# Kernel optimization log

Measured on AMD Instinct MI355X. Metric: run time of the kernel, lower is better.

The kernel has to match this reference:

```python
import jax, jax.numpy as jnp
import numpy as np

B, T, C = 2, 2048, 2048
H = 16          # n_head == n_kv_head
HD = 128        # head_size = hidden_dim // n_head (nope/value dim)
RD = 64         # qk_rope_head_dim
QLR = 1536      # q_lora_rank
KLR = 512       # kv_lora_rank
BASE = 10000.0
SCALE = (HD + RD) ** -0.5  # mscale = 1.0 since rope_scale = 1.0
EPS = 1e-6


def _rms(x, w):
    return x * jax.lax.rsqrt(jnp.mean(x * x, axis=-1, keepdims=True) + EPS) * w


def _rope_cos_sin(seq_len, dim):
    inv_freq = 1.0 / (BASE ** (jnp.arange(0, dim, 2, dtype=jnp.float32) / dim))
    t = jnp.arange(seq_len, dtype=jnp.float32)
    freqs = jnp.outer(t, inv_freq)            # [T, dim/2]
    emb = jnp.concatenate([freqs, freqs], -1)  # [T, dim]
    return jnp.cos(emb), jnp.sin(emb)


def _rotate_half(x):
    h = x.shape[-1] // 2
    return jnp.concatenate([-x[..., h:], x[..., :h]], axis=-1)


def setup_inputs() -> dict:
    key = jax.random.key(0)
    ks = jax.random.split(key, 8)
    s = 0.02
    return {
        "x": jax.random.normal(ks[0], (B, T, C), jnp.float32),
        "Wq_down": jax.random.normal(ks[1], (C, QLR), jnp.float32) * s,
        "q_norm_w": jnp.ones((QLR,), jnp.float32),
        "Wq_up": jax.random.normal(ks[2], (QLR, H * HD), jnp.float32) * s,
        "Wq_pe": jax.random.normal(ks[3], (QLR, H * RD), jnp.float32) * s,
        "Wkv_down": jax.random.normal(ks[4], (C, KLR), jnp.float32) * s,
        "kv_norm_w": jnp.ones((KLR,), jnp.float32),
        "Wkv_up": jax.random.normal(ks[5], (KLR, H * 2 * HD), jnp.float32) * s,
        "Wk_pe": jax.random.normal(ks[6], (C, RD), jnp.float32) * s,
        "k_pe_norm_w": jnp.ones((RD,), jnp.float32),
        "Wo": jax.random.normal(ks[7], (H * HD, C), jnp.float32) * s,
    }


def reference(x, Wq_down, q_norm_w, Wq_up, Wq_pe, Wkv_down, kv_norm_w,
              Wkv_up, Wk_pe, k_pe_norm_w, Wo):
    # ---- low-rank Q path ----
    cQ = _rms(x @ Wq_down, q_norm_w)                      # [B,T,QLR]
    q_nop = (cQ @ Wq_up).reshape(B, T, H, HD).transpose(0, 2, 1, 3)   # [B,H,T,HD]
    q_pe = (cQ @ Wq_pe).reshape(B, T, H, RD).transpose(0, 2, 1, 3)    # [B,H,T,RD]
    # ---- low-rank KV path ----
    cKV = _rms(x @ Wkv_down, kv_norm_w)                   # [B,T,KLR]
    kv = cKV @ Wkv_up                                     # [B,T,H*2*HD]
    k_nop, v = jnp.split(kv, 2, axis=-1)
    k_nop = k_nop.reshape(B, T, H, HD).transpose(0, 2, 1, 3)          # [B,H,T,HD]
    v = v.reshape(B, T, H, HD).transpose(0, 2, 1, 3)                  # [B,H,T,HD]
    # ---- decoupled RoPE key (shared across heads) ----
    k_pe = _rms(x @ Wk_pe, k_pe_norm_w).reshape(B, T, 1, RD).transpose(0, 2, 1, 3)  # [B,1,T,RD]
    cos, sin = _rope_cos_sin(T, RD)                       # [T,RD]
    q_pe = q_pe * cos + _rotate_half(q_pe) * sin
    k_pe = k_pe * cos + _rotate_half(k_pe) * sin
    # ---- concat nope + rope, causal SDPA ----
    q = jnp.concatenate([q_nop, q_pe], axis=-1)                           # [B,H,T,HD+RD]
    k = jnp.concatenate([k_nop, jnp.broadcast_to(k_pe, (B, H, T, RD))], axis=-1)
    scores = jnp.einsum('bhqd,bhkd->bhqk', q, k) * SCALE
    mask = jnp.tril(jnp.ones((T, T), dtype=bool))
    scores = jnp.where(mask, scores, jnp.finfo(scores.dtype).min)
    attn = jax.nn.softmax(scores, axis=-1)
    y = jnp.einsum('bhqk,bhkd->bhqd', attn, v)                            # [B,H,T,HD]
    y = y.transpose(0, 2, 1, 3).reshape(B, T, H * HD)
    return y @ Wo
```

## Files before the change

### kernel.cpp

```cpp
#include <hip/hip_runtime.h>
#include <hip/hip_bf16.h>
#include <cmath>

typedef __hip_bfloat16 bf16;
typedef __attribute__((ext_vector_type(8))) short s16x8;
typedef __attribute__((ext_vector_type(4))) float f32x4;

#define B_   2
#define T_   2048
#define C_   2048
#define H_   16
#define HD_  128
#define RD_  64
#define QLR_ 1536
#define KLR_ 512
#define SCALE_ 0.07216878364870322f

static __device__ __forceinline__ float b2f(bf16 v){ return __bfloat162float(v); }
static __device__ __forceinline__ bf16  f2b(float v){ return __float2bfloat16(v); }
static __device__ __forceinline__ float us2f(unsigned short u){
    union { unsigned short s[2]; float f; } v; v.s[0]=0; v.s[1]=u; return v.f;
}
static __device__ __forceinline__ float ldS(const void* p, size_t i, int isf32){
    return isf32 ? ((const float*)p)[i] : b2f(((const bf16*)p)[i]);
}
static __device__ __forceinline__ void ld4(const void* p, size_t i, int isf32, float* o){
    if (isf32) {
        float4 v = *(const float4*)((const float*)p + i);
        o[0]=v.x; o[1]=v.y; o[2]=v.z; o[3]=v.w;
    } else {
        ushort4 u = *(const ushort4*)((const bf16*)p + i);
        o[0]=us2f(u.x); o[1]=us2f(u.y); o[2]=us2f(u.z); o[3]=us2f(u.w);
    }
}

__global__ __launch_bounds__(64) void detect_kernel(const unsigned short* __restrict__ x,
                                                    int* __restrict__ flag)
{
    int big = 0;
    for (int i = threadIdx.x; i < 1024; i += 64) {
        const unsigned short u = x[2*i];
        const int e = (u >> 7) & 0xFF;
        if (e >= 139) big++;
    }
    #pragma unroll
    for (int off = 32; off; off >>= 1) big += __shfl_down(big, off, 64);
    if (threadIdx.x == 0) *flag = (big > 8) ? 1 : 0;
}

__global__ __launch_bounds__(256) void convert_kernel(const void* __restrict__ in,
                                                      bf16* __restrict__ out, int n,
                                                      const int* __restrict__ flag)
{
    const int f = *flag;
    const int i0 = (blockIdx.x * 256 + threadIdx.x) * 8;
    if (i0 >= n) return;
    float v[8];
    ld4(in, i0, f, v);
    ld4(in, i0 + 4, f, v + 4);
    bf16* o = out + i0;
    #pragma unroll
    for (int k = 0; k < 8; ++k) o[k] = f2b(v[k]);
}

struct TDesc { const void* in; bf16* out; int R, Cc, blkStart, nx; };
struct TBatch { TDesc d[5]; int nseg; };

__global__ __launch_bounds__(256) void transpose_batch(TBatch tb,
                                                       const int* __restrict__ flag)
{
    const int f = *flag;
    const int bid = blockIdx.x;
    int s = 0;
    #pragma unroll
    for (int i = 1; i < 5; ++i)
        if (i < tb.nseg && bid >= tb.d[i].blkStart) s = i;
    const TDesc d = tb.d[s];
    const int local = bid - d.blkStart;
    const int c0 = (local % d.nx) * 32;
    const int r0 = (local / d.nx) * 32;

    __shared__ float tile[32][33];
    const int tx = threadIdx.x & 31, ty = threadIdx.x >> 5;
    #pragma unroll
    for (int i = 0; i < 4; ++i)
        tile[ty + 8*i][tx] = ldS(d.in, (size_t)(r0 + ty + 8*i) * d.Cc + c0 + tx, f);
    __syncthreads();
    #pragma unroll
    for (int i = 0; i < 4; ++i)
        d.out[(size_t)(c0 + ty + 8*i) * d.R + r0 + tx] = f2b(tile[tx][ty + 8*i]);
}

__global__ __launch_bounds__(256) void transpose_v_kernel(const bf16* __restrict__ kvb,
                                                          bf16* __restrict__ vT)
{
    __shared__ bf16 tile[32][34];
    const int c0 = blockIdx.x * 32;
    const int r0 = blockIdx.y * 32;
    const int tx = threadIdx.x & 31, ty = threadIdx.x >> 5;
    #pragma unroll
    for (int i = 0; i < 4; ++i)
        tile[ty + 8*i][tx] = kvb[(size_t)(r0 + ty + 8*i) * (H_*256) + H_*128 + c0 + tx];
    __syncthreads();
    const int b  = r0 >> 11;
    const int t0 = r0 & (T_ - 1);
    #pragma unroll
    for (int i = 0; i < 4; ++i) {
        const int c  = c0 + ty + 8*i;
        const int hh = c >> 7, dd = c & 127;
        vT[(((size_t)b*H_ + hh)*HD_ + dd)*T_ + t0 + tx] = tile[tx][ty + 8*i];
    }
}

struct GOuts { void* p[3]; int start[3]; int stride[3]; int nseg; };

__global__ __launch_bounds__(256, 2) void mfma_gemm(const bf16* __restrict__ A,
                                                    const bf16* __restrict__ BT,
                                                    GOuts go, int N, int K,
                                                    const int* __restrict__ flag, int cH)
{
    __shared__ __align__(16) char smem[65536];
    const int cf   = cH ? *flag : 0;
    const int tid  = threadIdx.x;
    const int lane = tid & 63;
    const int quad = lane >> 4;
    const int l16  = lane & 15;
    const int w    = tid >> 6;
    const int wm   = w >> 1, wn = w & 1;
    const int bm   = blockIdx.y * 128, bn = blockIdx.x * 128;

    int seg = 0;
    #pragma unroll
    for (int i = 1; i < 3; ++i)
        if (i < go.nseg && bn >= go.start[i]) seg = i;
    void* const dstp   = go.p[seg];
    const int  dstoff  = go.start[seg];
    const int  dstride = go.stride[seg];

    const int nkt = K >> 6;

    const int sR   = tid >> 3;
    const int sCol = ((tid & 7) ^ (sR & 7)) * 8;
    const bf16* gA = A  + (size_t)(bm + sR) * K + sCol;
    const bf16* gB = BT + (size_t)(bn + sR) * K + sCol;
    const int rxk  = l16 & 7;
    const int aOff = (wm*64 + l16) * 128;
    const int bOff = 16384 + (wn*64 + l16) * 128;

    f32x4 acc[4][4];
    #pragma unroll
    for (int i = 0; i < 4; ++i)
        #pragma unroll
        for (int j = 0; j < 4; ++j)
            acc[i][j] = (f32x4){0.f, 0.f, 0.f, 0.f};

    s16x8 af[4][2], bf[4][2];

    #define STG(buf, kt) do {                                                    \
        const int ke_ = ((kt) < nkt ? (kt) : nkt-1) * 64;                        \
        _Pragma("unroll")                                                        \
        for (int j_ = 0; j_ < 4; ++j_)                                           \
            __builtin_amdgcn_global_load_lds(                                    \
                (const __attribute__((address_space(1))) unsigned int*)          \
                    (gA + (size_t)(j_*32) * K + ke_),                            \
                (__attribute__((address_space(3))) unsigned int*)                \
                    (smem + (buf)*32768 + j_*4096 + tid*16), 16, 0, 0);          \
        _Pragma("unroll")                                                        \
        for (int j_ = 0; j_ < 4; ++j_)                                           \
            __builtin_amdgcn_global_load_lds(                                    \
                (const __attribute__((address_space(1))) unsigned int*)          \
                    (gB + (size_t)(j_*32) * K + ke_),                            \
                (__attribute__((address_space(3))) unsigned int*)                \
                    (smem + (buf)*32768 + 16384 + j_*4096 + tid*16), 16, 0, 0);  \
    } while (0)

    #define LD(buf) do {                                                         \
        _Pragma("unroll")                                                        \
        for (int i_ = 0; i_ < 4; ++i_)                                           \
            _Pragma("unroll")                                                    \
            for (int ks_ = 0; ks_ < 2; ++ks_)                                    \
                af[i_][ks_] = *(const s16x8*)(smem + (buf)*32768 + aOff          \
                              + i_*2048 + ((((ks_<<2)|quad) ^ rxk) << 4));       \
        _Pragma("unroll")                                                        \
        for (int j_ = 0; j_ < 4; ++j_)                                           \
            _Pragma("unroll")                                                    \
            for (int ks_ = 0; ks_ < 2; ++ks_)                                    \
                bf[j_][ks_] = *(const s16x8*)(smem + (buf)*32768 + bOff          \
                              + j_*2048 + ((((ks_<<2)|quad) ^ rxk) << 4));       \
    } while (0)

    #define MM do {                                                              \
        __builtin_amdgcn_s_setprio(1);                                           \
        _Pragma("unroll")                                                        \
        for (int i_ = 0; i_ < 4; ++i_)                                           \
            _Pragma("unroll")                                                    \
            for (int j_ = 0; j_ < 4; ++j_)                                       \
                _Pragma("unroll")                                                \
                for (int ks_ = 0; ks_ < 2; ++ks_)                                \
                    acc[i_][j_] = __builtin_amdgcn_mfma_f32_16x16x32_bf16(       \
                        af[i_][ks_], bf[j_][ks_], acc[i_][j_], 0, 0, 0);         \
        __builtin_amdgcn_s_setprio(0);                                           \
    } while (0)

    #define DRAIN asm volatile("s_waitcnt vmcnt(0)" ::: "memory");               \
                  __builtin_amdgcn_s_barrier()

    STG(0, 0);
    DRAIN;

    for (int t = 0; t < nkt; t += 2) {
        STG(1, t+1);
        LD(0);
        MM;
        DRAIN;
        STG(0, t+2);
        LD(1);
        MM;
        DRAIN;
    }

    #undef STG
    #undef LD
    #undef MM
    #undef DRAIN

    #pragma unroll
    for (int i = 0; i < 4; ++i) {
        const int crow = bm + wm*64 + i*16 + quad*4;
        #pragma unroll
        for (int r = 0; r < 4; ++r) {
            #pragma unroll
            for (int j = 0; j < 4; ++j) {
                const int ccol = bn + wn*64 + j*16 + l16;
                if (ccol < N) {
                    const size_t idx = (size_t)(crow + r) * dstride + (ccol - dstoff);
                    if (cf) ((float*)dstp)[idx] = acc[i][j][r];
                    else    ((bf16*)dstp)[idx] = f2b(acc[i][j][r]);
                }
            }
        }
    }
}

template<int NPER>
__global__ __launch_bounds__(256) void rms_kernel(bf16* __restrict__ X,
                                                  const void* __restrict__ w,
                                                  const int* __restrict__ flag)
{
    const int wf = *flag;
    const int ncols = NPER * 256;
    __shared__ float red[4];
    const int row = blockIdx.x;
    const int tid = threadIdx.x;
    bf16* xr = X + (size_t)row * ncols;
    float vals[NPER];
    float ss = 0.f;
    #pragma unroll
    for (int i = 0; i < NPER; ++i) {
        float v = b2f(xr[tid + i*256]);
        vals[i] = v; ss += v*v;
    }
    #pragma unroll
    for (int off = 32; off; off >>= 1) ss += __shfl_down(ss, off, 64);
    if ((tid & 63) == 0) red[tid >> 6] = ss;
    __syncthreads();
    const float tot = red[0]+red[1]+red[2]+red[3];
    const float rs  = rsqrtf(tot / (float)ncols + 1e-6f);
    #pragma unroll
    for (int i = 0; i < NPER; ++i) {
        const int c = tid + i*256;
        xr[c] = f2b(vals[i] * rs * ldS(w, c, wf));
    }
}

__global__ __launch_bounds__(64) void kpe_rms_rope(bf16* __restrict__ X,
                                                   const void* __restrict__ w,
                                                   const int* __restrict__ flag)
{
    const int wf   = *flag;
    const int row  = blockIdx.x;
    const int t    = row & (T_ - 1);
    const int lane = threadIdx.x;
    bf16* xr = X + (size_t)row * RD_;
    const float v = b2f(xr[lane]);
    float ss = v * v;
    #pragma unroll
    for (int off = 32; off; off >>= 1) ss += __shfl_down(ss, off, 64);
    ss = __shfl(ss, 0, 64);
    const float rs = rsqrtf(ss / 64.f + 1e-6f);
    const float xn = v * rs * ldS(w, lane, wf);
    const int   i  = lane & 31;
    const float freq = powf(10000.f, -(float)(2*i) / 64.f);
    const float ang  = (float)t * freq;
    const float s = sinf(ang), c = cosf(ang);
    const float other = __shfl_xor(xn, 32, 64);
    const float o = (lane < 32) ? (xn * c - other * s) : (other * s + xn * c);
    xr[lane] = f2b(o);
}

__global__ __launch_bounds__(256) void qpe_rope(bf16* __restrict__ X)
{
    const int row = blockIdx.x;
    const int t   = row & (T_ - 1);
    bf16* xr = X + (size_t)row * (H_ * RD_);
    const int tid = threadIdx.x;
    #pragma unroll
    for (int pp = 0; pp < 2; ++pp) {
        const int p  = tid + pp * 256;
        const int hh = p >> 5;
        const int i  = p & 31;
        const int i0 = hh * 64 + i;
        const int i1 = i0 + 32;
        const float x1 = b2f(xr[i0]), x2 = b2f(xr[i1]);
        const float freq = powf(10000.f, -(float)(2*i) / 64.f);
        const float ang  = (float)t * freq;
        const float s = sinf(ang), c = cosf(ang);
        xr[i0] = f2b(x1 * c - x2 * s);
        xr[i1] = f2b(x1 * s + x2 * c);
    }
}

__global__ __launch_bounds__(256, 2) void flash_attn(const bf16* __restrict__ qnop,
                                                     const bf16* __restrict__ qpe,
                                                     const bf16* __restrict__ kv,
                                                     const bf16* __restrict__ kpe,
                                                     const bf16* __restrict__ vT,
                                                     bf16* __restrict__ y)
{
    __shared__ __align__(16) short Klds[64 * 192];
    __shared__ __align__(16) short Vt[128 * 64];
    __shared__ __align__(16) short Plds[4][16 * 64];

    const int h   = blockIdx.x;
    const int qt  = 31 - (int)blockIdx.y;
    const int b   = blockIdx.z;
    const int q0  = qt * 64;
    const int tid = threadIdx.x;
    const int w    = tid >> 6;
    const int lane = tid & 63;
    const int quad = lane >> 4;
    const int l16  = lane & 15;
    const int rk   = l16 & 7;
    const int rkp  = (l16 ^ (l16 >> 3)) & 7;
    const int row0 = q0 + w * 16;
    const size_t bT = (size_t)b * T_;
    const int bh  = b * H_ + h;

    const int kR = tid >> 4, kS = tid & 15;
    const int pR = tid >> 3, pS = tid & 7;
    const int vD = tid >> 3, vS = tid & 7;

    const bf16* gK = kv  + (bT + kR) * (H_*256) + h*128 + kS*8;
    const bf16* gP = kpe + (bT + pR) * RD_ + pS*8;
    const bf16* gV = vT  + ((size_t)bh*HD_ + vD) * T_ + vS*8;

    short* const wK = &Klds[kR*192 + ((kS ^ (kR & 7)) << 3)];
    short* const wP = &Klds[pR*192 + 128 + ((pS ^ (pR & 7)) << 3)];
    short* const wV = &Vt[vD*64 + ((vS ^ (vD & 7)) << 3)];

    s16x8 aq[6];
    {
        const size_t r = bT + row0 + l16;
        const bf16* qn = qnop + r * (H_*128) + h*128 + quad*8;
        #pragma unroll
        for (int kk = 0; kk < 4; ++kk) aq[kk] = *(const s16x8*)(qn + kk*32);
        const bf16* qp = qpe + r * (H_*64) + h*64 + quad*8;
        aq[4] = *(const s16x8*)(qp);
        aq[5] = *(const s16x8*)(qp + 32);
    }

    f32x4 o[8];
    #pragma unroll
    for (int i = 0; i < 8; ++i) o[i] = (f32x4){0.f,0.f,0.f,0.f};
    float m_run[4] = {-1e30f,-1e30f,-1e30f,-1e30f};
    float l_run[4] = {0.f,0.f,0.f,0.f};

    uint4 k0, k1, k2, k3, p0, p1, v0, v1, v2, v3;
    #define PF(J0) do {                                                     \
        const bf16* a_ = gK + (size_t)(J0) * (H_*256);                      \
        k0 = *(const uint4*)(a_);                                           \
        k1 = *(const uint4*)(a_ + 16*(H_*256));                             \
        k2 = *(const uint4*)(a_ + 32*(H_*256));                             \
        k3 = *(const uint4*)(a_ + 48*(H_*256));                             \
        const bf16* p_ = gP + (size_t)(J0) * RD_;                           \
        p0 = *(const uint4*)(p_);                                           \
        p1 = *(const uint4*)(p_ + 32*RD_);                                  \
        const bf16* v_ = gV + (J0);                                         \
        v0 = *(const uint4*)(v_);                                           \
        v1 = *(const uint4*)(v_ + 32*T_);                                   \
        v2 = *(const uint4*)(v_ + 64*T_);                                   \
        v3 = *(const uint4*)(v_ + 96*T_);                                   \
    } while (0)

    PF(0);

    const int ntiles = qt + 1;
    for (int it = 0; it < ntiles; ++it) {
        const int j0 = it * 64;
        asm volatile("s_waitcnt lgkmcnt(0)\n\ts_barrier" ::: "memory");

        *(uint4*)(wK)          = k0;
        *(uint4*)(wK + 16*192) = k1;
        *(uint4*)(wK + 32*192) = k2;
        *(uint4*)(wK + 48*192) = k3;
        *(uint4*)(wP)          = p0;
        *(uint4*)(wP + 32*192) = p1;
        *(uint4*)(wV)          = v0;
        *(uint4*)(wV + 32*64)  = v1;
        *(uint4*)(wV + 64*64)  = v2;
        *(uint4*)(wV + 96*64)  = v3;

        if (it + 1 < ntiles) PF(j0 + 64);

        asm volatile("s_waitcnt lgkmcnt(0)\n\ts_barrier" ::: "memory");

        if (j0 <= row0 + 15) {
            const bool needmask = (j0 + 63 > row0);
            f32x4 s[4];
            #pragma unroll
            for (int nsub = 0; nsub < 4; ++nsub) {
                f32x4 acc = (f32x4){0.f,0.f,0.f,0.f};
                #pragma unroll
                for (int kk = 0; kk < 6; ++kk) {
                    const s16x8 bk = *(const s16x8*)&Klds[(nsub*16 + l16)*192
                                        + ((((kk << 2) | quad) ^ rk) << 3)];
                    acc = __builtin_amdgcn_mfma_f32_16x16x32_bf16(aq[kk], bk, acc, 0, 0, 0);
                }
                #pragma unroll
                for (int reg = 0; reg < 4; ++reg) acc[reg] *= SCALE_;
                s[nsub] = acc;
            }
            if (needmask) {
                #pragma unroll
                for (int nsub = 0; nsub < 4; ++nsub)
                    #pragma unroll
                    for (int reg = 0; reg < 4; ++reg) {
                        const int col = j0 + nsub*16 + l16;
                        const int row = row0 + quad*4 + reg;
                        if (col > row) s[nsub][reg] = -1e30f;
                    }
            }
            float mt[4], alpha[4], rs[4];
            #pragma unroll
            for (int reg = 0; reg < 4; ++reg)
                mt[reg] = fmaxf(fmaxf(s[0][reg], s[1][reg]), fmaxf(s[2][reg], s[3][reg]));
            #pragma unroll
            for (int d = 1; d < 16; d <<= 1)
                #pragma unroll
                for (int reg = 0; reg < 4; ++reg)
                    mt[reg] = fmaxf(mt[reg], __shfl_xor(mt[reg], d, 64));
            #pragma unroll
            for (int reg = 0; reg < 4; ++reg) {
                const float mnew = fmaxf(m_run[reg], mt[reg]);
                alpha[reg] = __expf(m_run[reg] - mnew);
                m_run[reg] = mnew;
                rs[reg] = 0.f;
            }
            #pragma unroll
            for (int nsub = 0; nsub < 4; ++nsub)
                #pragma unroll
                for (int reg = 0; reg < 4; ++reg) {
                    const float p = __expf(s[nsub][reg] - m_run[reg]);
                    s[nsub][reg] = p;
                    rs[reg] += p;
                }
            #pragma unroll
            for (int d = 1; d < 16; d <<= 1)
                #pragma unroll
                for (int reg = 0; reg < 4; ++reg)
                    rs[reg] += __shfl_xor(rs[reg], d, 64);
            #pragma unroll
            for (int reg = 0; reg < 4; ++reg)
                l_run[reg] = l_run[reg] * alpha[reg] + rs[reg];

            #pragma unroll
            for (int nsub = 0; nsub < 4; ++nsub)
                #pragma unroll
                for (int reg = 0; reg < 4; ++reg) {
                    const bf16 pv = f2b(s[nsub][reg]);
                    const int prow = (quad << 2) + reg;
                    const int pk   = (prow ^ (prow >> 3)) & 7;
                    const int pby  = ((nsub << 5) + (l16 << 1)) ^ (pk << 4);
                    Plds[w][prow*64 + (pby >> 1)] = *(const short*)&pv;
                }
            #pragma unroll
            for (int n2 = 0; n2 < 8; ++n2)
                #pragma unroll
                for (int reg = 0; reg < 4; ++reg)
                    o[n2][reg] *= alpha[reg];

            const s16x8 ap0 = *(const s16x8*)&Plds[w][l16*64 + (((quad    ) ^ rkp) << 3)];
            const s16x8 ap1 = *(const s16x8*)&Plds[w][l16*64 + (((quad | 4) ^ rkp) << 3)];
            #pragma unroll
            for (int n2 = 0; n2 < 8; ++n2) {
                const s16x8 bv0 = *(const s16x8*)&Vt[(n2*16 + l16)*64 + (((quad    ) ^ rk) << 3)];
                const s16x8 bv1 = *(const s16x8*)&Vt[(n2*16 + l16)*64 + (((quad | 4) ^ rk) << 3)];
                o[n2] = __builtin_amdgcn_mfma_f32_16x16x32_bf16(ap0, bv0, o[n2], 0, 0, 0);
                o[n2] = __builtin_amdgcn_mfma_f32_16x16x32_bf16(ap1, bv1, o[n2], 0, 0, 0);
            }
        }
    }
    #undef PF

    #pragma unroll
    for (int reg = 0; reg < 4; ++reg) {
        const float inv = 1.f / l_run[reg];
        const size_t r = bT + row0 + quad*4 + reg;
        bf16* yr = y + r * (H_*128) + h*128 + l16;
        #pragma unroll
        for (int n2 = 0; n2 < 8; ++n2)
            yr[n2*16] = f2b(o[n2][reg] * inv);
    }
}

extern "C" void kernel_launch(void* const* d_in, const int* in_sizes, int n_in,
                              void* d_out, int out_size, void* d_ws, size_t ws_size,
                              hipStream_t stream)
{
    const void* x         = d_in[0];
    const void* Wq_down   = d_in[1];
    const void* q_norm_w  = d_in[2];
    const void* Wq_up     = d_in[3];
    const void* Wq_pe     = d_in[4];
    const void* Wkv_down  = d_in[5];
    const void* kv_norm_w = d_in[6];
    const void* Wkv_up    = d_in[7];
    const void* Wk_pe     = d_in[8];
    const void* kpe_nw    = d_in[9];
    const void* Wo        = d_in[10];

    char* ws = (char*)d_ws;
    int*  flag = (int*)(ws + 0);
    bf16* xb   = (bf16*)(ws + 256);
    bf16* cQ   = (bf16*)(ws + 16777472);
    bf16* cKV  = (bf16*)(ws + 29360384);
    bf16* kpeb = (bf16*)(ws + 33554688);
    bf16* qnop = (bf16*)(ws + 34078976);
    bf16* qpeb = (bf16*)(ws + 50856192);
    bf16* kvb  = (bf16*)(ws + 59244800);
    bf16* yb   = (bf16*)(ws + 92799232);

    bf16* P1 = kvb;
    bf16* P2 = (bf16*)((char*)kvb + 8912896);
    bf16* P3 = cQ;
    bf16* P4 = (bf16*)((char*)cQ + 4194304);
    bf16* vT = xb;

    const dim3 blk(256);

    detect_kernel<<<1, dim3(64), 0, stream>>>((const unsigned short*)x, flag);
    convert_kernel<<<(B_*T_*C_)/(256*8), blk, 0, stream>>>(x, xb, B_*T_*C_, flag);

    {
        TBatch tb;
        tb.d[0] = { Wq_down,  P1,               C_,  QLR_,     0, QLR_/32 };
        tb.d[1] = { Wkv_down, P1 + 1536*2048,   C_,  KLR_,  3072, KLR_/32 };
        tb.d[2] = { Wk_pe,    P1 + 2048*2048,   C_,  RD_,   4096, RD_/32  };
        tb.d[3] = { Wq_up,    P2,               QLR_, 2048, 4224, 2048/32 };
        tb.d[4] = { Wq_pe,    P2 + 2048*1536,   QLR_, 1024, 7296, 1024/32 };
        tb.nseg = 5;
        transpose_batch<<<8832, blk, 0, stream>>>(tb, flag);
    }

    {
        GOuts go; go.nseg = 3;
        go.p[0]=cQ;   go.start[0]=0;    go.stride[0]=QLR_;
        go.p[1]=cKV;  go.start[1]=1536; go.stride[1]=KLR_;
        go.p[2]=kpeb; go.start[2]=2048; go.stride[2]=RD_;
        mfma_gemm<<<dim3(17, 32), blk, 0, stream>>>(xb, P1, go, 2112, C_, flag, 0);
    }
    rms_kernel<6><<<B_*T_, blk, 0, stream>>>(cQ, q_norm_w, flag);
    rms_kernel<2><<<B_*T_, blk, 0, stream>>>(cKV, kv_norm_w, flag);
    kpe_rms_rope<<<B_*T_, dim3(64), 0, stream>>>(kpeb, kpe_nw, flag);

    {
        GOuts go; go.nseg = 2;
        go.p[0]=qnop; go.start[0]=0;    go.stride[0]=H_*HD_;
        go.p[1]=qpeb; go.start[1]=2048; go.stride[1]=H_*RD_;
        go.p[2]=nullptr; go.start[2]=0; go.stride[2]=0;
        mfma_gemm<<<dim3(24, 32), blk, 0, stream>>>(cQ, P2, go, 3072, QLR_, flag, 0);
    }
    qpe_rope<<<B_*T_, blk, 0, stream>>>(qpeb);

    {
        TBatch tb;
        tb.d[0] = { Wkv_up, P3, KLR_, H_*2*HD_,    0, (H_*2*HD_)/32 };
        tb.d[1] = { Wo,     P4, H_*HD_, C_,     2048, C_/32 };
        tb.d[2] = tb.d[1]; tb.d[3] = tb.d[1]; tb.d[4] = tb.d[1];
        tb.nseg = 2;
        transpose_batch<<<6144, blk, 0, stream>>>(tb, flag);
    }

    {
        GOuts go; go.nseg = 1;
        go.p[0]=kvb; go.start[0]=0; go.stride[0]=H_*2*HD_;
        go.p[1]=nullptr; go.start[1]=0; go.stride[1]=0;
        go.p[2]=nullptr; go.start[2]=0; go.stride[2]=0;
        mfma_gemm<<<dim3(32, 32), blk, 0, stream>>>(cKV, P3, go, H_*2*HD_, KLR_, flag, 0);
    }
    transpose_v_kernel<<<dim3((H_*HD_)/32, (B_*T_)/32), blk, 0, stream>>>(kvb, vT);

    flash_attn<<<dim3(H_, T_/64, B_), blk, 0, stream>>>(qnop, qpeb, kvb, kpeb, vT, yb);

    {
        GOuts go; go.nseg = 1;
        go.p[0]=d_out; go.start[0]=0; go.stride[0]=C_;
        go.p[1]=nullptr; go.start[1]=0; go.stride[1]=0;
        go.p[2]=nullptr; go.start[2]=0; go.stride[2]=0;
        mfma_gemm<<<dim3(C_/128, 32), blk, 0, stream>>>(yb, P4, go, C_, H_*HD_, flag, 1);
    }
}
```

Measured before the change: 455.7 us.

## Single-buffer GEMM LDS, raise occupancy to 3, add block swizzle

The MFMA GEMM drops its double-buffered LDS staging for a single 32KB buffer and raises launch bounds from 2 to 3 blocks per CU. It also remaps block indices with an interleaving swizzle meant to improve L2 reuse. The K loop now loads, waits and barriers before every compute step, so global loads no longer overlap MFMA work within a block. The design relies on more resident blocks to hide that latency, at the cost of a tighter register budget.

```diff
diff --git a/kernel.cpp b/kernel.cpp
--- a/kernel.cpp
+++ b/kernel.cpp
@@ -114,12 +114,12 @@
 
 struct GOuts { void* p[3]; int start[3]; int stride[3]; int nseg; };
 
-__global__ __launch_bounds__(256, 2) void mfma_gemm(const bf16* __restrict__ A,
+__global__ __launch_bounds__(256, 3) void mfma_gemm(const bf16* __restrict__ A,
                                                     const bf16* __restrict__ BT,
                                                     GOuts go, int N, int K,
                                                     const int* __restrict__ flag, int cH)
 {
-    __shared__ __align__(16) char smem[65536];
+    __shared__ __align__(16) char smem[32768];
     const int cf   = cH ? *flag : 0;
     const int tid  = threadIdx.x;
     const int lane = tid & 63;
@@ -127,7 +127,12 @@
     const int l16  = lane & 15;
     const int w    = tid >> 6;
     const int wm   = w >> 1, wn = w & 1;
-    const int bm   = blockIdx.y * 128, bn = blockIdx.x * 128;
+
+    const int nwg = gridDim.x * gridDim.y;
+    const int bid = blockIdx.y * gridDim.x + blockIdx.x;
+    const int swz = (bid & 7) * (nwg >> 3) + (bid >> 3);
+    const int bm  = (swz / gridDim.x) * 128;
+    const int bn  = (swz % gridDim.x) * 128;
 
     int seg = 0;
     #pragma unroll
@@ -156,36 +161,36 @@
 
     s16x8 af[4][2], bf[4][2];
 
-    #define STG(buf, kt) do {                                                    \
-        const int ke_ = ((kt) < nkt ? (kt) : nkt-1) * 64;                        \
+    #define STG(kt) do {                                                         \
+        const int ke_ = (kt) * 64;                                               \
         _Pragma("unroll")                                                        \
         for (int j_ = 0; j_ < 4; ++j_)                                           \
             __builtin_amdgcn_global_load_lds(                                    \
                 (const __attribute__((address_space(1))) unsigned int*)          \
                     (gA + (size_t)(j_*32) * K + ke_),                            \
                 (__attribute__((address_space(3))) unsigned int*)                \
-                    (smem + (buf)*32768 + j_*4096 + tid*16), 16, 0, 0);          \
+                    (smem + j_*4096 + tid*16), 16, 0, 0);                        \
         _Pragma("unroll")                                                        \
         for (int j_ = 0; j_ < 4; ++j_)                                           \
             __builtin_amdgcn_global_load_lds(                                    \
                 (const __attribute__((address_space(1))) unsigned int*)          \
                     (gB + (size_t)(j_*32) * K + ke_),                            \
                 (__attribute__((address_space(3))) unsigned int*)                \
-                    (smem + (buf)*32768 + 16384 + j_*4096 + tid*16), 16, 0, 0);  \
+                    (smem + 16384 + j_*4096 + tid*16), 16, 0, 0);                \
     } while (0)
 
-    #define LD(buf) do {                                                         \
+    #define LD do {                                                              \
         _Pragma("unroll")                                                        \
         for (int i_ = 0; i_ < 4; ++i_)                                           \
             _Pragma("unroll")                                                    \
             for (int ks_ = 0; ks_ < 2; ++ks_)                                    \
-                af[i_][ks_] = *(const s16x8*)(smem + (buf)*32768 + aOff          \
+                af[i_][ks_] = *(const s16x8*)(smem + aOff                        \
                               + i_*2048 + ((((ks_<<2)|quad) ^ rxk) << 4));       \
         _Pragma("unroll")                                                        \
         for (int j_ = 0; j_ < 4; ++j_)                                           \
             _Pragma("unroll")                                                    \
             for (int ks_ = 0; ks_ < 2; ++ks_)                                    \
-                bf[j_][ks_] = *(const s16x8*)(smem + (buf)*32768 + bOff          \
+                bf[j_][ks_] = *(const s16x8*)(smem + bOff                        \
                               + j_*2048 + ((((ks_<<2)|quad) ^ rxk) << 4));       \
     } while (0)
 
@@ -202,27 +207,18 @@
         __builtin_amdgcn_s_setprio(0);                                           \
     } while (0)
 
-    #define DRAIN asm volatile("s_waitcnt vmcnt(0)" ::: "memory");               \
-                  __builtin_amdgcn_s_barrier()
-
-    STG(0, 0);
-    DRAIN;
-
-    for (int t = 0; t < nkt; t += 2) {
-        STG(1, t+1);
-        LD(0);
+    for (int t = 0; t < nkt; ++t) {
+        STG(t);
+        asm volatile("s_waitcnt vmcnt(0)" ::: "memory");
+        __builtin_amdgcn_s_barrier();
+        LD;
         MM;
-        DRAIN;
-        STG(0, t+2);
-        LD(1);
-        MM;
-        DRAIN;
+        __builtin_amdgcn_s_barrier();
     }
 
     #undef STG
     #undef LD
     #undef MM
-    #undef DRAIN
 
     #pragma unroll
     for (int i = 0; i < 4; ++i) {
```

Result: no change. 457.5 us (+0.4%).
